# Performance work log

Measured on AMD Instinct MI355X. Metric: run time of the kernel, lower is better.

Reference implementation:

```python
import jax, jax.numpy as jnp
import numpy as np

BINS = 256
H = 2048
N = 2_000_000


def _tensor2image(x):
    # standard GAN denorm: [-1,1] -> [0,1]
    return (x + 1.0) * 0.5


def _cdf(vals):
    # torch.histc(bins=256, min=0, max=256): unit-width bins, values in [0,255]
    idx = jnp.clip(jnp.floor(vals), 0, BINS - 1).astype(jnp.int32)
    hist = jnp.zeros((BINS,), jnp.float32).at[idx].add(1.0)
    return jnp.cumsum(hist) / hist.sum()


def _trans_table(ref_cdf, adj_cdf):
    # cal_trans: for i in 1..255, first j in 1..255 with adj[j-1] <= ref[i] <= adj[j]
    i_vals = ref_cdf[1:]  # [255]
    cond = (adj_cdf[:-1][None, :] <= i_vals[:, None]) & (i_vals[:, None] <= adj_cdf[1:][None, :])  # [255,255]
    found = cond.any(axis=1)
    first_j = jnp.argmax(cond, axis=1) + 1
    tab = jnp.where(found, first_j, jnp.arange(1, BINS))  # unmatched entries keep identity
    tab = jnp.concatenate([jnp.zeros((1,), tab.dtype), tab])
    tab = tab.at[BINS - 1].set(BINS - 1)
    return tab.astype(jnp.float32)


def _hist_match(dst_img, ref_img, i0, i1, i2, i3):
    # dst_img, ref_img: [3,H,W]; indices: [N]
    dst_align = dst_img[:, i0, i1]  # [3,N]
    ref_align = ref_img[:, i2, i3]  # [3,N]
    cdf_dst = jax.vmap(_cdf)(dst_align)  # [3,256]
    cdf_ref = jax.vmap(_cdf)(ref_align)  # [3,256]
    tables = jax.vmap(_trans_table)(cdf_dst, cdf_ref)  # [3,256]
    bins = jnp.clip(dst_align, 0, BINS - 1).astype(jnp.int32)  # int() truncation on [0,255]
    new_align = jnp.take_along_axis(tables, bins, axis=1)  # [3,N]
    return dst_img.at[:, i0, i1].set(new_align)


def reference(input_data, target_data, mask_src, mask_tar, index0, index1, index2, index3, ref_data):
    inp = _tensor2image(input_data) * 255.0
    tgt = _tensor2image(target_data) * 255.0
    ref = _tensor2image(ref_data) * 255.0
    h = mask_src.shape[2]
    m_src = jnp.broadcast_to(mask_src, (1, 3, h, h))
    m_tar = jnp.broadcast_to(mask_tar, (1, 3, h, h))
    input_masked = inp * m_src
    target_masked = (tgt * m_tar)[0]  # [3,H,W]
    ref_masked = (ref * m_src)[0]     # [3,H,W]
    i0, i1, i2, i3 = index0[0], index1[0], index2[0], index3[0]
    matched = _hist_match(ref_masked, target_masked, i0, i1, i2, i3)[None]  # [1,3,H,W]
    input_match = jax.lax.stop_gradient(matched) * m_src  # no_grad in original
    return jnp.mean((input_masked - input_match) ** 2)


def setup_inputs() -> dict:
    key = jax.random.key(0)
    ks = jax.random.split(key, 9)
    inp = {
        "input_data": jax.random.uniform(ks[0], (1, 3, H, H), jnp.float32, -1.0, 1.0),
        "target_data": jax.random.uniform(ks[1], (1, 3, H, H), jnp.float32, -1.0, 1.0),
        "mask_src": (jax.random.uniform(ks[2], (1, 1, H, H)) > 0.5).astype(jnp.float32),
        "mask_tar": (jax.random.uniform(ks[3], (1, 1, H, H)) > 0.5).astype(jnp.float32),
        "index0": jax.random.randint(ks[4], (1, N), 0, H, jnp.int32),
        "index1": jax.random.randint(ks[5], (1, N), 0, H, jnp.int32),
        "index2": jax.random.randint(ks[6], (1, N), 0, H, jnp.int32),
        "index3": jax.random.randint(ks[7], (1, N), 0, H, jnp.int32),
        "ref_data": jax.random.uniform(ks[8], (1, 3, H, H), jnp.float32, -1.0, 1.0),
    }
    return inp
```

## Files before the change

### kernel.cpp

```cpp
#include <hip/hip_runtime.h>

#define HDIM 2048
#define HH (HDIM * HDIM)
#define NIDX 2000000
#define BINS 256
#define NCOPY 16
#define TL_BLOCKS 2048
#define HIST_BLOCKS 2048

#define PART_OFF     0
#define TAB_OFF      16384
#define HIST_OFF     20480
#define PACKED_D_OFF 1048576
#define PACKED_R_OFF 17825792

__global__ __launch_bounds__(256) void pack_kernel(
    const float* __restrict__ ref, const float* __restrict__ tgt,
    const float* __restrict__ msrc, const float* __restrict__ mtar,
    unsigned* __restrict__ packed_d, unsigned* __restrict__ packed_r,
    unsigned* __restrict__ hist)
{
    const int gtid = blockIdx.x * 256 + threadIdx.x;
    const int stride = gridDim.x * 256;

    for (int k = gtid; k < NCOPY * 6 * BINS; k += stride) hist[k] = 0;

    for (int g = gtid; g < HH / 4; g += stride) {
        const int p = g * 4;
        const float4 ms4 = *(const float4*)(msrc + p);
        const float4 mt4 = *(const float4*)(mtar + p);
        const float ms[4] = {ms4.x, ms4.y, ms4.z, ms4.w};
        const float mt[4] = {mt4.x, mt4.y, mt4.z, mt4.w};
        unsigned od[4] = {0, 0, 0, 0}, orr[4] = {0, 0, 0, 0};
#pragma unroll
        for (int c = 0; c < 3; c++) {
            const float4 rv = *(const float4*)(ref + c * HH + p);
            const float4 tv = *(const float4*)(tgt + c * HH + p);
            const float r[4] = {rv.x, rv.y, rv.z, rv.w};
            const float tt[4] = {tv.x, tv.y, tv.z, tv.w};
#pragma unroll
            for (int k = 0; k < 4; k++) {
                const float vd = ((r[k] + 1.0f) * 0.5f) * 255.0f * ms[k];
                const float vr = ((tt[k] + 1.0f) * 0.5f) * 255.0f * mt[k];
                const unsigned bd = (unsigned)(int)fminf(fmaxf(floorf(vd), 0.0f), 255.0f);
                const unsigned br = (unsigned)(int)fminf(fmaxf(floorf(vr), 0.0f), 255.0f);
                od[k]  |= bd << (8 * c);
                orr[k] |= br << (8 * c);
            }
        }
        *(uint4*)(packed_d + p) = make_uint4(od[0], od[1], od[2], od[3]);
        *(uint4*)(packed_r + p) = make_uint4(orr[0], orr[1], orr[2], orr[3]);
    }
}

__global__ __launch_bounds__(256) void hist_kernel(
    unsigned* __restrict__ packed_d, const unsigned* __restrict__ packed_r,
    const int* __restrict__ i0, const int* __restrict__ i1,
    const int* __restrict__ i2, const int* __restrict__ i3,
    unsigned* __restrict__ hist)
{
    __shared__ unsigned lhist[6 * BINS];
    for (int k = threadIdx.x; k < 6 * BINS; k += 256) lhist[k] = 0;
    __syncthreads();

    unsigned z0 = 0, z1 = 0, z2 = 0, z3 = 0, z4 = 0, z5 = 0;
    unsigned char* sampled = (unsigned char*)packed_d;

    const int stride = gridDim.x * 256;
    for (int q = blockIdx.x * 256 + threadIdx.x; q < NIDX / 4; q += stride) {
        const int4 a = ((const int4*)i0)[q];
        const int4 b = ((const int4*)i1)[q];
        const int4 c = ((const int4*)i2)[q];
        const int4 d = ((const int4*)i3)[q];
        const int pd[4] = {a.x * HDIM + b.x, a.y * HDIM + b.y, a.z * HDIM + b.z, a.w * HDIM + b.w};
        const int pr[4] = {c.x * HDIM + d.x, c.y * HDIM + d.y, c.z * HDIM + d.z, c.w * HDIM + d.w};
        unsigned wd[4], wr[4];
#pragma unroll
        for (int k = 0; k < 4; k++) wd[k] = packed_d[pd[k]];
#pragma unroll
        for (int k = 0; k < 4; k++) wr[k] = packed_r[pr[k]];
#pragma unroll
        for (int k = 0; k < 4; k++) sampled[pd[k] * 4 + 3] = 1;
#pragma unroll
        for (int k = 0; k < 4; k++) {
            const unsigned d0 =  wd[k]        & 255u;
            const unsigned d1 = (wd[k] >> 8 ) & 255u;
            const unsigned d2 = (wd[k] >> 16) & 255u;
            const unsigned r0 =  wr[k]        & 255u;
            const unsigned r1 = (wr[k] >> 8 ) & 255u;
            const unsigned r2 = (wr[k] >> 16) & 255u;
            if (d0) atomicAdd(&lhist[           d0], 1u); else z0++;
            if (d1) atomicAdd(&lhist[1 * BINS + d1], 1u); else z1++;
            if (d2) atomicAdd(&lhist[2 * BINS + d2], 1u); else z2++;
            if (r0) atomicAdd(&lhist[3 * BINS + r0], 1u); else z3++;
            if (r1) atomicAdd(&lhist[4 * BINS + r1], 1u); else z4++;
            if (r2) atomicAdd(&lhist[5 * BINS + r2], 1u); else z5++;
        }
    }
    if (z0) atomicAdd(&lhist[0 * BINS], z0);
    if (z1) atomicAdd(&lhist[1 * BINS], z1);
    if (z2) atomicAdd(&lhist[2 * BINS], z2);
    if (z3) atomicAdd(&lhist[3 * BINS], z3);
    if (z4) atomicAdd(&lhist[4 * BINS], z4);
    if (z5) atomicAdd(&lhist[5 * BINS], z5);
    __syncthreads();
    unsigned* h = hist + (blockIdx.x & (NCOPY - 1)) * (6 * BINS);
    for (int k = threadIdx.x; k < 6 * BINS; k += 256) {
        const unsigned v = lhist[k];
        if (v) atomicAdd(&h[k], v);
    }
}

__global__ __launch_bounds__(256) void table_kernel(
    const unsigned* __restrict__ hist, float* __restrict__ tabg)
{
    __shared__ float    cdf[6 * BINS];
    __shared__ unsigned wsum[4];

    const int t    = threadIdx.x;
    const int lane = t & 63;
    const int wid  = t >> 6;

    for (int ch = 0; ch < 6; ch++) {
        unsigned x = 0;
#pragma unroll
        for (int cp = 0; cp < NCOPY; cp++) x += hist[cp * (6 * BINS) + ch * BINS + t];
#pragma unroll
        for (int d = 1; d < 64; d <<= 1) {
            const unsigned y = __shfl_up(x, d, 64);
            if (lane >= d) x += y;
        }
        if (lane == 63) wsum[wid] = x;
        __syncthreads();
        unsigned prefix = 0;
        for (int w = 0; w < wid; w++) prefix += wsum[w];
        x += prefix;
        cdf[ch * BINS + t] = (float)x / 2000000.0f;
        __syncthreads();
    }
    for (int c = 0; c < 3; c++) {
        float o;
        if (t == 0)             o = 0.0f;
        else if (t == BINS - 1) o = 255.0f;
        else {
            const float v = cdf[c * BINS + t];
            const float* arr = cdf + (3 + c) * BINS;
            int lo = 0, hi = 256;
            while (lo < hi) { const int mid = (lo + hi) >> 1; if (arr[mid] < v) lo = mid + 1; else hi = mid; }
            const int J0 = ((lo > 1) ? lo : 1) - 1;
            int lo2 = 0, hi2 = 256;
            while (lo2 < hi2) { const int mid = (lo2 + hi2) >> 1; if (arr[mid] <= v) lo2 = mid + 1; else hi2 = mid; }
            const int J1 = ((lo2 - 1) < 254 ? (lo2 - 1) : 254);
            const bool found = (lo2 >= 1) && (J0 <= J1);
            o = found ? (float)(J0 + 1) : (float)t;
        }
        tabg[c * BINS + t] = o;
    }
}

__global__ __launch_bounds__(256) void tabloss_kernel(
    const float* __restrict__ inp, const float* __restrict__ ref,
    const float* __restrict__ msrc, const float* __restrict__ tabg,
    const unsigned* __restrict__ packed_d, double* __restrict__ partials)
{
    __shared__ float  tab[3 * BINS];
    __shared__ double red[256];

    const int t = threadIdx.x;
    for (int k = t; k < 3 * BINS; k += 256) tab[k] = tabg[k];
    __syncthreads();

    double local = 0.0;
    const int stride = gridDim.x * 256;
    for (int g = blockIdx.x * 256 + t; g < HH / 4; g += stride) {
        const int p = g * 4;
        const float4 mv = *(const float4*)(msrc + p);
        const uint4 pw = *(const uint4*)(packed_d + p);
        const unsigned samp[4] = {pw.x >> 24, pw.y >> 24, pw.z >> 24, pw.w >> 24};
        const float m[4] = {mv.x, mv.y, mv.z, mv.w};
#pragma unroll
        for (int c = 0; c < 3; c++) {
            const float4 rv = *(const float4*)(ref + c * HH + p);
            const float4 iv = *(const float4*)(inp + c * HH + p);
            const float r[4] = {rv.x, rv.y, rv.z, rv.w};
            const float x4[4] = {iv.x, iv.y, iv.z, iv.w};
            float s = 0.0f;
#pragma unroll
            for (int k = 0; k < 4; k++) {
                const float mm = m[k];
                const float refm = ((r[k] + 1.0f) * 0.5f) * 255.0f * mm;
                const float inpm = ((x4[k] + 1.0f) * 0.5f) * 255.0f * mm;
                float matchv;
                if (samp[k]) {
                    const int bidx = (int)fminf(fmaxf(refm, 0.0f), 255.0f);
                    matchv = tab[c * BINS + bidx];
                } else {
                    matchv = refm;
                }
                const float dd = inpm - matchv * mm;
                s += dd * dd;
            }
            local += (double)s;
        }
    }
    red[t] = local;
    __syncthreads();
    for (int s2 = 128; s2 > 0; s2 >>= 1) {
        if (t < s2) red[t] += red[t + s2];
        __syncthreads();
    }
    if (t == 0) partials[blockIdx.x] = red[0];
}

__global__ __launch_bounds__(256) void finalize_kernel(
    const double* __restrict__ partials, float* __restrict__ out)
{
    const int t = threadIdx.x;
    double s = 0.0;
    for (int k = t; k < TL_BLOCKS; k += 256) s += partials[k];
    __shared__ double red[256];
    red[t] = s;
    __syncthreads();
    for (int s2 = 128; s2 > 0; s2 >>= 1) {
        if (t < s2) red[t] += red[t + s2];
        __syncthreads();
    }
    if (t == 0) out[0] = (float)(red[0] / (double)(3 * HH));
}

extern "C" void kernel_launch(void* const* d_in, const int* in_sizes, int n_in,
                              void* d_out, int out_size, void* d_ws, size_t ws_size,
                              hipStream_t stream)
{
    const float* input_data  = (const float*)d_in[0];
    const float* target_data = (const float*)d_in[1];
    const float* mask_src    = (const float*)d_in[2];
    const float* mask_tar    = (const float*)d_in[3];
    const int*   i0          = (const int*)d_in[4];
    const int*   i1          = (const int*)d_in[5];
    const int*   i2          = (const int*)d_in[6];
    const int*   i3          = (const int*)d_in[7];
    const float* ref_data    = (const float*)d_in[8];
    float* out = (float*)d_out;

    char* ws = (char*)d_ws;
    double*   partials = (double*)(ws + PART_OFF);
    float*    tabg     = (float*)(ws + TAB_OFF);
    unsigned* hist     = (unsigned*)(ws + HIST_OFF);
    unsigned* packed_d = (unsigned*)(ws + PACKED_D_OFF);
    unsigned* packed_r = (unsigned*)(ws + PACKED_R_OFF);

    pack_kernel<<<2048, 256, 0, stream>>>(ref_data, target_data, mask_src, mask_tar,
                                          packed_d, packed_r, hist);
    hist_kernel<<<HIST_BLOCKS, 256, 0, stream>>>(packed_d, packed_r, i0, i1, i2, i3, hist);
    table_kernel<<<1, 256, 0, stream>>>(hist, tabg);
    tabloss_kernel<<<TL_BLOCKS, 256, 0, stream>>>(input_data, ref_data, mask_src, tabg,
                                                  packed_d, partials);
    finalize_kernel<<<1, 256, 0, stream>>>(partials, out);
}
```

Before: 346.9 us.

## Window random gathers into cache-sized address ranges for histogram pass

The histogram kernel now processes the random gathers in 8 passes, each touching only one 2 MB window of the packed image (pd>>19 selects the window), and splits the dst and ref gathers into separate phases. The aim is to keep each pass's random-access footprint small enough to stay in L2/MALL cache and cut DRAM traffic from scattered 4-byte reads. In exchange, the index arrays are re-read 8 times per phase, and the added branching leaves many lanes of each wavefront idle.

Measured after the change: 371.7 us. +7.1%, slower.

```diff
diff --git a/kernel.cpp b/kernel.cpp
--- a/kernel.cpp
+++ b/kernel.cpp
@@ -6,7 +6,8 @@
 #define BINS 256
 #define NCOPY 16
 #define TL_BLOCKS 2048
-#define HIST_BLOCKS 2048
+#define WH_BLOCKS 2048
+#define NWIN 8
 
 #define PART_OFF     0
 #define TAB_OFF      16384
@@ -53,7 +54,7 @@
     }
 }
 
-__global__ __launch_bounds__(256) void hist_kernel(
+__global__ __launch_bounds__(256) void whist_kernel(
     unsigned* __restrict__ packed_d, const unsigned* __restrict__ packed_r,
     const int* __restrict__ i0, const int* __restrict__ i1,
     const int* __restrict__ i2, const int* __restrict__ i3,
@@ -65,38 +66,50 @@
 
     unsigned z0 = 0, z1 = 0, z2 = 0, z3 = 0, z4 = 0, z5 = 0;
     unsigned char* sampled = (unsigned char*)packed_d;
-
     const int stride = gridDim.x * 256;
-    for (int q = blockIdx.x * 256 + threadIdx.x; q < NIDX / 4; q += stride) {
-        const int4 a = ((const int4*)i0)[q];
-        const int4 b = ((const int4*)i1)[q];
-        const int4 c = ((const int4*)i2)[q];
-        const int4 d = ((const int4*)i3)[q];
-        const int pd[4] = {a.x * HDIM + b.x, a.y * HDIM + b.y, a.z * HDIM + b.z, a.w * HDIM + b.w};
-        const int pr[4] = {c.x * HDIM + d.x, c.y * HDIM + d.y, c.z * HDIM + d.z, c.w * HDIM + d.w};
-        unsigned wd[4], wr[4];
-#pragma unroll
-        for (int k = 0; k < 4; k++) wd[k] = packed_d[pd[k]];
-#pragma unroll
-        for (int k = 0; k < 4; k++) wr[k] = packed_r[pr[k]];
-#pragma unroll
-        for (int k = 0; k < 4; k++) sampled[pd[k] * 4 + 3] = 1;
-#pragma unroll
-        for (int k = 0; k < 4; k++) {
-            const unsigned d0 =  wd[k]        & 255u;
-            const unsigned d1 = (wd[k] >> 8 ) & 255u;
-            const unsigned d2 = (wd[k] >> 16) & 255u;
-            const unsigned r0 =  wr[k]        & 255u;
-            const unsigned r1 = (wr[k] >> 8 ) & 255u;
-            const unsigned r2 = (wr[k] >> 16) & 255u;
-            if (d0) atomicAdd(&lhist[           d0], 1u); else z0++;
-            if (d1) atomicAdd(&lhist[1 * BINS + d1], 1u); else z1++;
-            if (d2) atomicAdd(&lhist[2 * BINS + d2], 1u); else z2++;
-            if (r0) atomicAdd(&lhist[3 * BINS + r0], 1u); else z3++;
-            if (r1) atomicAdd(&lhist[4 * BINS + r1], 1u); else z4++;
-            if (r2) atomicAdd(&lhist[5 * BINS + r2], 1u); else z5++;
-        }
-    }
+
+    for (int w = 0; w < NWIN; w++) {
+        for (int q = blockIdx.x * 256 + threadIdx.x; q < NIDX / 4; q += stride) {
+            const int4 a = ((const int4*)i0)[q];
+            const int4 b = ((const int4*)i1)[q];
+            const int pd[4] = {a.x * HDIM + b.x, a.y * HDIM + b.y,
+                               a.z * HDIM + b.z, a.w * HDIM + b.w};
+#pragma unroll
+            for (int k = 0; k < 4; k++) {
+                if ((pd[k] >> 19) == w) {
+                    const unsigned wd = packed_d[pd[k]];
+                    sampled[pd[k] * 4 + 3] = 1;
+                    const unsigned d0 =  wd        & 255u;
+                    const unsigned d1 = (wd >> 8 ) & 255u;
+                    const unsigned d2 = (wd >> 16) & 255u;
+                    if (d0) atomicAdd(&lhist[           d0], 1u); else z0++;
+                    if (d1) atomicAdd(&lhist[1 * BINS + d1], 1u); else z1++;
+                    if (d2) atomicAdd(&lhist[2 * BINS + d2], 1u); else z2++;
+                }
+            }
+        }
+    }
+    for (int w = 0; w < NWIN; w++) {
+        for (int q = blockIdx.x * 256 + threadIdx.x; q < NIDX / 4; q += stride) {
+            const int4 c = ((const int4*)i2)[q];
+            const int4 d = ((const int4*)i3)[q];
+            const int pr[4] = {c.x * HDIM + d.x, c.y * HDIM + d.y,
+                               c.z * HDIM + d.z, c.w * HDIM + d.w};
+#pragma unroll
+            for (int k = 0; k < 4; k++) {
+                if ((pr[k] >> 19) == w) {
+                    const unsigned wr = packed_r[pr[k]];
+                    const unsigned r0 =  wr        & 255u;
+                    const unsigned r1 = (wr >> 8 ) & 255u;
+                    const unsigned r2 = (wr >> 16) & 255u;
+                    if (r0) atomicAdd(&lhist[3 * BINS + r0], 1u); else z3++;
+                    if (r1) atomicAdd(&lhist[4 * BINS + r1], 1u); else z4++;
+                    if (r2) atomicAdd(&lhist[5 * BINS + r2], 1u); else z5++;
+                }
+            }
+        }
+    }
+
     if (z0) atomicAdd(&lhist[0 * BINS], z0);
     if (z1) atomicAdd(&lhist[1 * BINS], z1);
     if (z2) atomicAdd(&lhist[2 * BINS], z2);
@@ -252,7 +265,7 @@
 
     pack_kernel<<<2048, 256, 0, stream>>>(ref_data, target_data, mask_src, mask_tar,
                                           packed_d, packed_r, hist);
-    hist_kernel<<<HIST_BLOCKS, 256, 0, stream>>>(packed_d, packed_r, i0, i1, i2, i3, hist);
+    whist_kernel<<<WH_BLOCKS, 256, 0, stream>>>(packed_d, packed_r, i0, i1, i2, i3, hist);
     table_kernel<<<1, 256, 0, stream>>>(hist, tabg);
     tabloss_kernel<<<TL_BLOCKS, 256, 0, stream>>>(input_data, ref_data, mask_src, tabg,
                                                   packed_d, partials);
```
